# Kernel tuning notes

Hardware: AMD Instinct MI355X
Metric: run time of the kernel (lower is better)

Reference implementation:

```python
import jax, jax.numpy as jnp
import numpy as np

D = 256      # feature_dim (d_model)
H = 4        # num_heads
N = 4096     # query nodes
M = 4096     # source nodes


def _conv1x1(W, b, x):
    # Conv1d(kernel_size=1): per-position linear over channels. x: [1, Cin, N]
    return jnp.einsum('oi,bin->bon', W, x) + b[None, :, None]


def setup_inputs() -> dict:
    key = jax.random.key(0)
    ks = jax.random.split(key, 16)
    s = 0.02
    inp = {
        'x':      jax.random.normal(ks[0], (1, D, N), jnp.float32),
        'source': jax.random.normal(ks[1], (1, D, M), jnp.float32),
        'dist':   jax.random.uniform(ks[2], (1, N, M), jnp.float32),
        'mask':   jax.random.bernoulli(ks[3], 0.5, (N, M)),
        'Wq': s * jax.random.normal(ks[4], (D, D), jnp.float32),  'bq': jnp.zeros((D,), jnp.float32),
        'Wk': s * jax.random.normal(ks[5], (D, D), jnp.float32),  'bk': jnp.zeros((D,), jnp.float32),
        'Wv': s * jax.random.normal(ks[6], (D, D), jnp.float32),  'bv': jnp.zeros((D,), jnp.float32),
        'Wm': s * jax.random.normal(ks[7], (D, D), jnp.float32),  'bm': jnp.zeros((D,), jnp.float32),
        'W1': s * jax.random.normal(ks[8], (2 * D, 2 * D), jnp.float32), 'b1': jnp.zeros((2 * D,), jnp.float32),
        'W2': s * jax.random.normal(ks[9], (D, 2 * D), jnp.float32),     'b2': jnp.zeros((D,), jnp.float32),
    }
    return inp


def reference(x, source, dist, mask, Wq, bq, Wk, bk, Wv, bv, Wm, bm, W1, b1, W2, b2):
    dim = D // H  # per-head dim; torch view(1, dim, H, -1) splits channels as (dim, H)
    q = _conv1x1(Wq, bq, x).reshape(1, dim, H, N)
    k = _conv1x1(Wk, bk, source).reshape(1, dim, H, M)
    v = _conv1x1(Wv, bv, source).reshape(1, dim, H, M)

    scores = jnp.einsum('bdhn,bdhm->bhnm', q, k) / jnp.sqrt(jnp.asarray(dim, q.dtype))
    # non-standard additive mask: global detached min scales the masked-out entries
    smin = jax.lax.stop_gradient(scores.min())
    scores = scores + smin * (~mask).astype(scores.dtype)[None, None, :, :]

    prob = jax.nn.softmax(scores, axis=-1)                       # [1,H,N,M]
    attn = jnp.einsum('bhnm,bdhm->bdhn', prob, v)                # [1,dim,H,N]
    message = _conv1x1(Wm, bm, attn.reshape(1, D, N))            # merge heads

    h = jnp.concatenate([x, message], axis=1)                    # [1,2D,N]
    h = jax.nn.relu(_conv1x1(W1, b1, h))
    y = _conv1x1(W2, b2, h)                                      # [1,D,N]
    weights = scores.mean(axis=1)                                # [1,N,M]
    return y, weights
```

## Files before the change

kernel.cpp:

```cpp
#include <hip/hip_runtime.h>
#include <hip/hip_bf16.h>
#include <math.h>

#define Dm 256
#define Hh 4
#define Nn 4096
#define Mq 4096

typedef __attribute__((ext_vector_type(8))) short bf16x8;
typedef __attribute__((ext_vector_type(4))) float f32x4;
typedef _Float16 __attribute__((ext_vector_type(4))) f16x4;

#define MFMA_BF16(a,b,c) __builtin_amdgcn_mfma_f32_16x16x32_bf16(a,b,c,0,0,0)
#define MFMA_F16x16(a,b,c) __builtin_amdgcn_mfma_f32_16x16x16f16(a,b,c,0,0,0)

#define MB (1u<<20)
#define OFF_FLAG  0
#define OFF_SMIN  64
#define OFF_PART  128
#define OFF_MT    4096
#define OFF_DENP  (128u<<10)
#define OFF_STATS (512u<<10)
#define OFF_WB    (3u*MB/2)
#define OFF_BITS  (3u*MB)
#define OFF_QB    (5u*MB)
#define OFF_KB    (7u*MB)
#define OFF_VB    (9u*MB)
#define OFF_HCAT  (11u*MB)
#define OFF_ATTNT (15u*MB)
#define OFF_XT    (17u*MB)
#define OFF_ST    (19u*MB)
#define OFF_OPART (17u*MB)
#define OFF_H1T   (17u*MB)

#define WOFF_Q  0
#define WOFF_K  65536
#define WOFF_V  131072
#define WOFF_M  196608
#define WOFF_1  262144
#define WOFF_2  524288

__device__ __forceinline__ unsigned short f2bf(float x) {
    unsigned u = __float_as_uint(x);
    u += 0x7FFF + ((u >> 16) & 1);
    return (unsigned short)(u >> 16);
}
__device__ __forceinline__ float bf2f(unsigned short b) {
    return __uint_as_float(((unsigned)b) << 16);
}

__global__ void k_detect(const unsigned char* __restrict__ mb, int* __restrict__ flag) {
    __shared__ int c[5];
    if (threadIdx.x < 5) c[threadIdx.x] = 0;
    __syncthreads();
    for (int i = threadIdx.x; i < 16384; i += blockDim.x) {
        unsigned char b = mb[i];
        if (b) {
            atomicAdd(&c[i & 3], 1);
            if ((i & 7) == 4) atomicAdd(&c[4], 1);
        }
    }
    __syncthreads();
    if (threadIdx.x == 0) {
        int f;
        if (c[3] > 0 && c[0] == 0)          f = 3;
        else if (c[1] | c[2] | c[3])        f = 1;
        else if (c[4] > 0)                  f = 0;
        else                                f = 2;
        *flag = f;
    }
}

__global__ void k_maskbits(const void* __restrict__ mp, const int* __restrict__ flagp,
                           unsigned char* __restrict__ bits) {
    size_t i = (size_t)blockIdx.x * 256 + threadIdx.x;
    const int flag = *flagp;
    size_t base = i * 8;
    unsigned b = 0;
    if (flag == 1) {
        unsigned long long u = *(const unsigned long long*)((const unsigned char*)mp + base);
        #pragma unroll
        for (int j = 0; j < 8; j++) b |= (unsigned)(((u >> (8*j)) & 0xFFull) != 0ull) << j;
    } else if (flag == 0) {
        const int* p = (const int*)mp;
        #pragma unroll
        for (int j = 0; j < 8; j++) b |= (unsigned)(p[base + j] != 0) << j;
    } else if (flag == 3) {
        const float* p = (const float*)mp;
        #pragma unroll
        for (int j = 0; j < 8; j++) b |= (unsigned)(p[base + j] != 0.0f) << j;
    } else {
        const unsigned long long* p = (const unsigned long long*)mp;
        #pragma unroll
        for (int j = 0; j < 8; j++) b |= (unsigned)(p[base + j] != 0ull) << j;
    }
    bits[i] = (unsigned char)b;
}

__global__ __launch_bounds__(256) void k_prep(const float* __restrict__ src,
                                              unsigned short* __restrict__ dst,
                                              unsigned short* __restrict__ dst2) {
    const int l = threadIdx.x & 63, g = threadIdx.x >> 6;
    const int c = blockIdx.y * 64 + l;
    const int n0 = blockIdx.x * 32 + g * 8;
    float4 v0 = *(const float4*)(src + (size_t)c * Nn + n0);
    float4 v1 = *(const float4*)(src + (size_t)c * Nn + n0 + 4);
    float vv[8] = {v0.x, v0.y, v0.z, v0.w, v1.x, v1.y, v1.z, v1.w};
    #pragma unroll
    for (int j = 0; j < 8; j++) {
        unsigned short b = f2bf(vv[j]);
        dst[(size_t)(n0 + j) * 256 + c] = b;
        if (dst2) dst2[(size_t)(n0 + j) * 512 + c] = b;
    }
}

__global__ void k_wcast(const float* __restrict__ Wq, const float* __restrict__ Wk,
                        const float* __restrict__ Wv, const float* __restrict__ Wm,
                        const float* __restrict__ W1, const float* __restrict__ W2,
                        unsigned short* __restrict__ wb) {
    size_t i = (size_t)blockIdx.x * 256 + threadIdx.x;
    const float* s; size_t off;
    if      (i < 65536)               { s = Wq; off = i; }
    else if (i < 131072)              { s = Wk; off = i - 65536; }
    else if (i < 196608)              { s = Wv; off = i - 131072; }
    else if (i < 262144)              { s = Wm; off = i - 196608; }
    else if (i < 524288)              { s = W1; off = i - 262144; }
    else                              { s = W2; off = i - 524288; }
    wb[i] = f2bf(s[off]);
}

template<int KK>
__device__ __forceinline__ void gemm_body(const unsigned short* __restrict__ wb,
                                          const float* __restrict__ bias,
                                          const unsigned short* __restrict__ xt,
                                          void* __restrict__ out, int mode,
                                          int bx, int by) {
    const int tid = threadIdx.x, w = tid >> 6, lane = tid & 63;
    const int lg = lane >> 4, lr = lane & 15;
    const int o_base = by * 64 + w * 16;
    const int n_base = bx * 64;
    f32x4 acc[4];
    #pragma unroll
    for (int j = 0; j < 4; j++) acc[j] = (f32x4){0.f, 0.f, 0.f, 0.f};
    const unsigned short* wrow = wb + (size_t)(o_base + lr) * KK + lg * 8;
    const unsigned short* xrow = xt + (size_t)(n_base + lr) * KK + lg * 8;
    #pragma unroll
    for (int k0 = 0; k0 < KK; k0 += 32) {
        bf16x8 af = *(const bf16x8*)(wrow + k0);
        #pragma unroll
        for (int j = 0; j < 4; j++) {
            bf16x8 bfr = *(const bf16x8*)(xrow + (size_t)j * 16 * KK + k0);
            acc[j] = MFMA_BF16(af, bfr, acc[j]);
        }
    }
    float bv[4];
    #pragma unroll
    for (int r = 0; r < 4; r++) bv[r] = bias[o_base + lg * 4 + r];
    #pragma unroll
    for (int j = 0; j < 4; j++) {
        #pragma unroll
        for (int r = 0; r < 4; r++) {
            int o = o_base + lg * 4 + r;
            int n = n_base + j * 16 + lr;
            float v = acc[j][r] + bv[r];
            if (mode == 0) {
                ((float*)out)[(size_t)o * Nn + n] = v;
            } else if (mode == 1) {
                ((unsigned short*)out)[(((size_t)(o & 3)) * Nn + n) * 64 + (o >> 2)] = f2bf(v);
            } else if (mode == 2) {
                union { _Float16 h; unsigned short u; } cv; cv.h = (_Float16)v;
                ((unsigned short*)out)[(((size_t)(o & 3)) * 64 + (o >> 2)) * Mq + n] = cv.u;
            } else if (mode == 3) {
                ((unsigned short*)out)[(size_t)n * 512 + 256 + o] = f2bf(v);
            } else if (mode == 4) {
                ((unsigned short*)out)[(size_t)n * 512 + o] = f2bf(fmaxf(v, 0.f));
            } else {
                int dd = o >> 2, hh = o & 3, g = dd >> 3, pos = dd & 7;
                int slot = g ^ (n & 7);
                ((unsigned short*)out)[(((size_t)hh * Mq + n)) * 64 + slot * 8 + pos] = f2bf(v);
            }
        }
    }
}

template<int KK>
__global__ __launch_bounds__(256) void k_mgemm(const unsigned short* __restrict__ wb,
                                               const float* __restrict__ bias,
                                               const unsigned short* __restrict__ xt,
                                               void* __restrict__ out, int mode) {
    gemm_body<KK>(wb, bias, xt, out, mode, blockIdx.x, blockIdx.y);
}

__global__ __launch_bounds__(256) void k_qkv(const unsigned short* __restrict__ wb,
                                             const float* __restrict__ bq,
                                             const float* __restrict__ bk,
                                             const float* __restrict__ bv,
                                             const unsigned short* __restrict__ xt,
                                             const unsigned short* __restrict__ st,
                                             void* __restrict__ qb, void* __restrict__ kb,
                                             void* __restrict__ vb) {
    const int z = blockIdx.z;
    const float* bias = (z == 0) ? bq : ((z == 1) ? bk : bv);
    const unsigned short* X = (z == 0) ? xt : st;
    void* out = (z == 0) ? qb : ((z == 1) ? kb : vb);
    int mode = (z == 0) ? 1 : ((z == 1) ? 5 : 2);
    gemm_body<256>(wb + z * 65536, bias, X, out, mode, blockIdx.x, blockIdx.y);
}

template<int PHASE>
__global__ __launch_bounds__(512) void k_score(
    const unsigned short* __restrict__ qb, const unsigned short* __restrict__ kb,
    const unsigned long long* __restrict__ bits,
    const float* __restrict__ sminp,
    float* __restrict__ stats, float* __restrict__ partial,
    float* __restrict__ wout) {
    __shared__ unsigned short kbuf[2][8192];
    const int tid = threadIdx.x;
    const int w = tid >> 6, lane = tid & 63;
    const int lg = lane >> 4, lr = lane & 15;
    const int n0 = blockIdx.x * 128 + w * 16;
    const int mb = blockIdx.y;
    const int m0 = mb * 512;

    bf16x8 qf[4][2];
    #pragma unroll
    for (int h = 0; h < 4; h++)
        #pragma unroll
        for (int kh = 0; kh < 2; kh++)
            qf[h][kh] = *(const bf16x8*)(qb + (((size_t)h * Nn + n0 + lr) << 6) + kh*32 + lg*8);

    float smin = 0.f;
    if (PHASE) smin = *sminp;

    const int h0 = tid >> 8, q0 = tid & 255;
    const unsigned short* src0 = kb + (((size_t)h0 * Mq + m0) << 6) + q0 * 8;
    const unsigned short* src1 = kb + (((size_t)(h0 + 2) * Mq + m0) << 6) + q0 * 8;
    unsigned short* dst0 = &kbuf[0][h0 * 2048 + q0 * 8];
    unsigned short* dst1 = &kbuf[0][(h0 + 2) * 2048 + q0 * 8];

    float mn = INFINITY;
    float mx1[4], mx0[4];
    #pragma unroll
    for (int h = 0; h < 4; h++) { mx1[h] = -INFINITY; mx0[h] = -INFINITY; }

    const unsigned long long* brow = bits + (((size_t)(n0 + lr)) << 6) + (m0 >> 6);
    unsigned long long bw = 0ull;

    bf16x8 r0 = *(const bf16x8*)(src0);
    bf16x8 r1 = *(const bf16x8*)(src1);
    *(bf16x8*)dst0 = r0;
    *(bf16x8*)dst1 = r1;
    __syncthreads();
    r0 = *(const bf16x8*)(src0 + 2048);
    r1 = *(const bf16x8*)(src1 + 2048);

    for (int t = 0; t < 16; t++) {
        const unsigned short* kB = &kbuf[t & 1][0];
        const int mch = m0 + t * 32;
        if ((t & 1) == 0) bw = brow[t >> 1];
        #pragma unroll
        for (int mi = 0; mi < 2; mi++) {
            const int rowoff = (mi * 16 + lr) * 64;
            const int shb = (t & 1) * 32 + mi * 16 + lg * 4;
            f32x4 ssum = (f32x4){0.f, 0.f, 0.f, 0.f};
            #pragma unroll
            for (int h = 0; h < 4; h++) {
                bf16x8 a0 = *(const bf16x8*)(kB + h*2048 + rowoff + ((lg ^ (lr & 7)) << 3));
                bf16x8 a1 = *(const bf16x8*)(kB + h*2048 + rowoff + (((lg + 4) ^ (lr & 7)) << 3));
                f32x4 acc = (f32x4){0.f, 0.f, 0.f, 0.f};
                acc = MFMA_BF16(a0, qf[h][0], acc);
                acc = MFMA_BF16(a1, qf[h][1], acc);
                if (PHASE == 0) {
                    #pragma unroll
                    for (int r = 0; r < 4; r++) {
                        float v = acc[r] * 0.125f;
                        mn = fminf(mn, v);
                        bool b = (bw >> (shb + r)) & 1ull;
                        mx1[h] = fmaxf(mx1[h], b ? v : -INFINITY);
                        mx0[h] = fmaxf(mx0[h], b ? -INFINITY : v);
                    }
                } else {
                    ssum += acc;
                }
            }
            if (PHASE == 1) {
                f32x4 wv;
                #pragma unroll
                for (int r = 0; r < 4; r++) {
                    bool b = (bw >> (shb + r)) & 1ull;
                    wv[r] = ssum[r] * 0.03125f + (b ? 0.f : smin);
                }
                *(f32x4*)(wout + (size_t)(n0 + lr) * Mq + mch + mi * 16 + lg * 4) = wv;
            }
        }
        if (t < 15) {
            *(bf16x8*)(dst0 + (((t + 1) & 1) ? 8192 : 0)) = r0;
            *(bf16x8*)(dst1 + (((t + 1) & 1) ? 8192 : 0)) = r1;
        }
        __syncthreads();
        if (t < 14) {
            r0 = *(const bf16x8*)(src0 + (size_t)(t + 2) * 2048);
            r1 = *(const bf16x8*)(src1 + (size_t)(t + 2) * 2048);
        }
    }

    if (PHASE == 0) {
        #pragma unroll
        for (int h = 0; h < 4; h++) {
            mx1[h] = fmaxf(mx1[h], __shfl_xor(mx1[h], 16));
            mx1[h] = fmaxf(mx1[h], __shfl_xor(mx1[h], 32));
            mx0[h] = fmaxf(mx0[h], __shfl_xor(mx0[h], 16));
            mx0[h] = fmaxf(mx0[h], __shfl_xor(mx0[h], 32));
        }
        if (lane < 16) {
            #pragma unroll
            for (int h = 0; h < 4; h++) {
                size_t row = (size_t)h * Nn + n0 + lane;
                stats[row * 16 + mb * 2 + 0] = mx1[h];
                stats[row * 16 + mb * 2 + 1] = mx0[h];
            }
        }
        for (int off = 1; off < 64; off <<= 1) mn = fminf(mn, __shfl_xor(mn, off));
        __shared__ float wmin[8];
        if (lane == 0) wmin[w] = mn;
        __syncthreads();
        if (tid == 0) {
            float m2 = wmin[0];
            #pragma unroll
            for (int i = 1; i < 8; i++) m2 = fminf(m2, wmin[i]);
            partial[blockIdx.x * 8 + mb] = m2;
        }
    }
}

__global__ void k_minreduce(const float* __restrict__ partial, float* __restrict__ smin) {
    const int tid = threadIdx.x;
    float mn = partial[tid];
    __shared__ float red[256];
    red[tid] = mn;
    __syncthreads();
    for (int st = 128; st > 0; st >>= 1) {
        if (tid < st) red[tid] = fminf(red[tid], red[tid + st]);
        __syncthreads();
    }
    if (tid == 0) *smin = red[0];
}

__global__ void k_rowfix(const float* __restrict__ stats, const float* __restrict__ sminp,
                         float* __restrict__ mtarr) {
    int row = blockIdx.x * 256 + threadIdx.x;
    float smin = *sminp;
    float mt = -INFINITY;
    #pragma unroll
    for (int mb = 0; mb < 8; mb++) {
        float a = stats[(size_t)row * 16 + mb * 2];
        float b = stats[(size_t)row * 16 + mb * 2 + 1];
        mt = fmaxf(mt, fmaxf(a, b + smin));
    }
    mtarr[row] = mt;
}

__global__ __launch_bounds__(512) void k_pv(
    const unsigned short* __restrict__ qb, const unsigned short* __restrict__ kb,
    const unsigned short* __restrict__ vbh,
    const unsigned long long* __restrict__ bits,
    const float* __restrict__ sminp, const float* __restrict__ mtarr,
    float* __restrict__ denp, unsigned short* __restrict__ opart) {
    __shared__ unsigned short kbuf[2][4096];
    const int tid = threadIdx.x;
    const int w = tid >> 6, lane = tid & 63;
    const int lg = lane >> 4, lr = lane & 15;
    const int h = blockIdx.y & 3, mb = (blockIdx.y >> 2) & 3, dh = blockIdx.y >> 4;
    const int n0 = blockIdx.x * 512 + w * 64;
    const int m0 = mb * 1024;
    const float smin = *sminp;

    bf16x8 qf[4][2];
    float mt[4];
    #pragma unroll
    for (int ns = 0; ns < 4; ns++) {
        #pragma unroll
        for (int kh = 0; kh < 2; kh++)
            qf[ns][kh] = *(const bf16x8*)(qb + (((size_t)h * Nn + n0 + ns*16 + lr) << 6) + kh*32 + lg*8);
        mt[ns] = mtarr[(size_t)h * Nn + n0 + ns*16 + lr];
    }

    f32x4 oacc[4][2];
    float dsum[4];
    #pragma unroll
    for (int ns = 0; ns < 4; ns++) {
        oacc[ns][0] = (f32x4){0.f,0.f,0.f,0.f};
        oacc[ns][1] = (f32x4){0.f,0.f,0.f,0.f};
        dsum[ns] = 0.f;
    }

    const unsigned short* ksrc = kb + (((size_t)h * Mq + m0) << 6) + tid * 8;
    bf16x8 r0 = *(const bf16x8*)(ksrc);
    *(bf16x8*)&kbuf[0][tid * 8] = r0;
    __syncthreads();
    r0 = *(const bf16x8*)(ksrc + 4096);

    const unsigned short* vrow0 = vbh + ((size_t)(h * 64 + dh * 32 + lr)) * Mq;
    const unsigned short* vrow1 = vbh + ((size_t)(h * 64 + dh * 32 + 16 + lr)) * Mq;

    for (int t = 0; t < 16; t++) {
        const unsigned short* kB = &kbuf[t & 1][0];
        const int mch = m0 + t * 64;
        unsigned long long bw[4];
        #pragma unroll
        for (int ns = 0; ns < 4; ns++)
            bw[ns] = bits[(((size_t)(n0 + ns*16 + lr)) << 6) + (mch >> 6)];
        #pragma unroll
        for (int mi = 0; mi < 4; mi++) {
            const int rowoff = (mi * 16 + lr) * 64;
            bf16x8 a0 = *(const bf16x8*)(kB + rowoff + ((lg ^ (lr & 7)) << 3));
            bf16x8 a1 = *(const bf16x8*)(kB + rowoff + (((lg + 4) ^ (lr & 7)) << 3));
            f16x4 vf0 = *(const f16x4*)(vrow0 + mch + mi * 16 + lg * 4);
            f16x4 vf1 = *(const f16x4*)(vrow1 + mch + mi * 16 + lg * 4);
            const int shb = mi * 16 + lg * 4;
            #pragma unroll
            for (int ns = 0; ns < 4; ns++) {
                f32x4 acc = (f32x4){0.f,0.f,0.f,0.f};
                acc = MFMA_BF16(a0, qf[ns][0], acc);
                acc = MFMA_BF16(a1, qf[ns][1], acc);
                f16x4 pf;
                float dloc = 0.f;
                #pragma unroll
                for (int r = 0; r < 4; r++) {
                    bool b = (bw[ns] >> (shb + r)) & 1ull;
                    float v = acc[r] * 0.125f + (b ? 0.f : smin);
                    float p = __expf(v - mt[ns]);
                    dloc += p;
                    pf[r] = (_Float16)p;
                }
                dsum[ns] += dloc;
                oacc[ns][0] = MFMA_F16x16(pf, vf0, oacc[ns][0]);
                oacc[ns][1] = MFMA_F16x16(pf, vf1, oacc[ns][1]);
            }
        }
        if (t < 15) *(bf16x8*)&kbuf[(t + 1) & 1][tid * 8] = r0;
        __syncthreads();
        if (t < 14) r0 = *(const bf16x8*)(ksrc + (size_t)(t + 2) * 4096);
    }

    #pragma unroll
    for (int ns = 0; ns < 4; ns++) {
        dsum[ns] += __shfl_xor(dsum[ns], 16);
        dsum[ns] += __shfl_xor(dsum[ns], 32);
    }
    if (dh == 0 && lane < 16) {
        #pragma unroll
        for (int ns = 0; ns < 4; ns++)
            denp[((size_t)h * Nn + n0 + ns*16 + lane) * 4 + mb] = dsum[ns];
    }
    unsigned short* op = opart + (size_t)mb * (Dm * Nn);
    #pragma unroll
    for (int ns = 0; ns < 4; ns++)
        #pragma unroll
        for (int ds = 0; ds < 2; ds++) {
            int c = (dh * 32 + ds * 16 + lr) * 4 + h;
            int n = n0 + ns * 16 + lg * 4;
            unsigned long long pk =
                (unsigned long long)f2bf(oacc[ns][ds][0]) |
                ((unsigned long long)f2bf(oacc[ns][ds][1]) << 16) |
                ((unsigned long long)f2bf(oacc[ns][ds][2]) << 32) |
                ((unsigned long long)f2bf(oacc[ns][ds][3]) << 48);
            *(unsigned long long*)&op[(size_t)c * Nn + n] = pk;
        }
}

__global__ __launch_bounds__(256) void k_finish(const unsigned short* __restrict__ opart,
                                                const float* __restrict__ denp,
                                                unsigned short* __restrict__ attnT) {
    __shared__ float t[64][65];
    const int cb = blockIdx.y * 64, nb = blockIdx.x * 64;
    const int tid = threadIdx.x;
    #pragma unroll
    for (int e = 0; e < 16; e++) {
        int idx = e * 256 + tid;
        int c_l = idx >> 6, n_l = idx & 63;
        int c = cb + c_l, n = nb + n_l;
        float s = 0.f;
        #pragma unroll
        for (int y = 0; y < 4; y++)
            s += bf2f(opart[(size_t)y * (Dm*Nn) + (size_t)c * Nn + n]);
        size_t row = (size_t)(c & 3) * Nn + n;
        float d = denp[row*4] + denp[row*4+1] + denp[row*4+2] + denp[row*4+3];
        t[c_l][n_l] = s / d;
    }
    __syncthreads();
    #pragma unroll
    for (int e = 0; e < 16; e++) {
        int idx = e * 256 + tid;
        int n_l = idx >> 6, c_l = idx & 63;
        attnT[(size_t)(nb + n_l) * 256 + cb + c_l] = f2bf(t[c_l][n_l]);
    }
}

extern "C" void kernel_launch(void* const* d_in, const int* in_sizes, int n_in,
                              void* d_out, int out_size, void* d_ws, size_t ws_size,
                              hipStream_t stream) {
    const float* x      = (const float*)d_in[0];
    const float* source = (const float*)d_in[1];
    const void*  mask   = d_in[3];
    const float* Wq = (const float*)d_in[4];  const float* bq = (const float*)d_in[5];
    const float* Wk = (const float*)d_in[6];  const float* bk = (const float*)d_in[7];
    const float* Wv = (const float*)d_in[8];  const float* bv = (const float*)d_in[9];
    const float* Wm = (const float*)d_in[10]; const float* bm = (const float*)d_in[11];
    const float* W1 = (const float*)d_in[12]; const float* b1 = (const float*)d_in[13];
    const float* W2 = (const float*)d_in[14]; const float* b2 = (const float*)d_in[15];

    float* y    = (float*)d_out;
    float* wout = y + (size_t)Dm * Nn;

    char* ws = (char*)d_ws;
    int*   flag  = (int*)(ws + OFF_FLAG);
    float* sminp = (float*)(ws + OFF_SMIN);
    float* part  = (float*)(ws + OFF_PART);
    float* mtarr = (float*)(ws + OFF_MT);
    float* denp  = (float*)(ws + OFF_DENP);
    float* stats = (float*)(ws + OFF_STATS);
    unsigned short* wb    = (unsigned short*)(ws + OFF_WB);
    unsigned char*  bits  = (unsigned char*)(ws + OFF_BITS);
    unsigned short* qb    = (unsigned short*)(ws + OFF_QB);
    unsigned short* kb    = (unsigned short*)(ws + OFF_KB);
    unsigned short* vb    = (unsigned short*)(ws + OFF_VB);
    unsigned short* hcat  = (unsigned short*)(ws + OFF_HCAT);
    unsigned short* attnT = (unsigned short*)(ws + OFF_ATTNT);
    unsigned short* xt    = (unsigned short*)(ws + OFF_XT);
    unsigned short* st    = (unsigned short*)(ws + OFF_ST);
    unsigned short* opart = (unsigned short*)(ws + OFF_OPART);
    unsigned short* h1t   = (unsigned short*)(ws + OFF_H1T);

    k_detect<<<1, 256, 0, stream>>>((const unsigned char*)mask, flag);
    k_maskbits<<<8192, 256, 0, stream>>>(mask, flag, bits);

    k_prep<<<dim3(128, 4), 256, 0, stream>>>(x, xt, hcat);
    k_prep<<<dim3(128, 4), 256, 0, stream>>>(source, st, nullptr);
    k_wcast<<<2560, 256, 0, stream>>>(Wq, Wk, Wv, Wm, W1, W2, wb);

    k_qkv<<<dim3(64, 4, 3), 256, 0, stream>>>(wb, bq, bk, bv, xt, st, qb, kb, vb);

    k_score<0><<<dim3(32, 8), 512, 0, stream>>>(qb, kb, (const unsigned long long*)bits,
                                                nullptr, stats, part, nullptr);
    k_minreduce<<<1, 256, 0, stream>>>(part, sminp);
    k_rowfix<<<64, 256, 0, stream>>>(stats, sminp, mtarr);

    k_score<1><<<dim3(32, 8), 512, 0, stream>>>(qb, kb, (const unsigned long long*)bits,
                                                sminp, nullptr, nullptr, wout);

    k_pv<<<dim3(8, 32), 512, 0, stream>>>(qb, kb, vb, (const unsigned long long*)bits,
                                          sminp, mtarr, denp, opart);
    k_finish<<<dim3(64, 4), 256, 0, stream>>>(opart, denp, attnT);

    k_mgemm<256><<<dim3(64, 4), 256, 0, stream>>>(wb + WOFF_M, bm, attnT, hcat, 3);
    k_mgemm<512><<<dim3(64, 8), 256, 0, stream>>>(wb + WOFF_1, b1, hcat, h1t, 4);
    k_mgemm<512><<<dim3(64, 4), 256, 0, stream>>>(wb + WOFF_2, b2, h1t, y, 0);
}
```

Measured before the change: 235.3 us.

## Replace exact row max with Cauchy-Schwarz bound and stage V in LDS

The exact per-row softmax max is no longer computed from masked score statistics. It is replaced by a Cauchy-Schwarz upper bound, |q|·max|k|/8 plus a clamped smin, computed by small norm kernels. This removes the stats output and the row-fix kernel and makes the min pass lighter. The PV kernel is restructured to stage V tiles through double-buffered LDS, cover all 64 head dims per block, and fold scale and offset into an exp2 FMA. The bound may underflow exponents when it is loose, which trades accuracy risk for fewer passes over the score matrix.

```diff
diff --git a/kernel.cpp b/kernel.cpp
--- a/kernel.cpp
+++ b/kernel.cpp
@@ -18,9 +18,9 @@
 #define OFF_FLAG  0
 #define OFF_SMIN  64
 #define OFF_PART  128
+#define OFF_KMAX  2048
 #define OFF_MT    4096
 #define OFF_DENP  (128u<<10)
-#define OFF_STATS (512u<<10)
 #define OFF_WB    (3u*MB/2)
 #define OFF_BITS  (3u*MB)
 #define OFF_QB    (5u*MB)
@@ -207,20 +207,49 @@
     gemm_body<256>(wb + z * 65536, bias, X, out, mode, blockIdx.x, blockIdx.y);
 }
 
-template<int PHASE>
-__global__ __launch_bounds__(512) void k_score(
+__global__ void k_init(unsigned* __restrict__ kmax) {
+    if (threadIdx.x < 4) kmax[threadIdx.x] = 0u;
+}
+
+__global__ __launch_bounds__(256) void k_knorm(const unsigned short* __restrict__ kb,
+                                               unsigned* __restrict__ kmax) {
+    const int h = blockIdx.y;
+    const int m = blockIdx.x * 256 + threadIdx.x;
+    const unsigned short* row = kb + ((size_t)(h * Mq + m) << 6);
+    float s = 0.f;
+    #pragma unroll
+    for (int i = 0; i < 64; i++) { float v = bf2f(row[i]); s = fmaf(v, v, s); }
+    __shared__ float red[256];
+    red[threadIdx.x] = s;
+    __syncthreads();
+    for (int st = 128; st > 0; st >>= 1) {
+        if (threadIdx.x < st) red[threadIdx.x] = fmaxf(red[threadIdx.x], red[threadIdx.x + st]);
+        __syncthreads();
+    }
+    if (threadIdx.x == 0) atomicMax(kmax + h, __float_as_uint(red[0]));
+}
+
+__global__ __launch_bounds__(256) void k_qnorm(const unsigned short* __restrict__ qb,
+                                               const unsigned* __restrict__ kmax,
+                                               float* __restrict__ mtarr) {
+    const int row = blockIdx.x * 256 + threadIdx.x;
+    const unsigned short* qr = qb + ((size_t)row << 6);
+    float s = 0.f;
+    #pragma unroll
+    for (int i = 0; i < 64; i++) { float v = bf2f(qr[i]); s = fmaf(v, v, s); }
+    float k2 = __uint_as_float(kmax[row >> 12]);
+    mtarr[row] = sqrtf(s * k2) * 0.125f;
+}
+
+__global__ __launch_bounds__(512) void k_min(
     const unsigned short* __restrict__ qb, const unsigned short* __restrict__ kb,
-    const unsigned long long* __restrict__ bits,
-    const float* __restrict__ sminp,
-    float* __restrict__ stats, float* __restrict__ partial,
-    float* __restrict__ wout) {
+    float* __restrict__ partial) {
     __shared__ unsigned short kbuf[2][8192];
     const int tid = threadIdx.x;
     const int w = tid >> 6, lane = tid & 63;
     const int lg = lane >> 4, lr = lane & 15;
     const int n0 = blockIdx.x * 128 + w * 16;
-    const int mb = blockIdx.y;
-    const int m0 = mb * 512;
+    const int m0 = blockIdx.y * 512;
 
     bf16x8 qf[4][2];
     #pragma unroll
@@ -228,9 +257,6 @@
         #pragma unroll
         for (int kh = 0; kh < 2; kh++)
             qf[h][kh] = *(const bf16x8*)(qb + (((size_t)h * Nn + n0 + lr) << 6) + kh*32 + lg*8);
-
-    float smin = 0.f;
-    if (PHASE) smin = *sminp;
 
     const int h0 = tid >> 8, q0 = tid & 255;
     const unsigned short* src0 = kb + (((size_t)h0 * Mq + m0) << 6) + q0 * 8;
@@ -239,12 +265,6 @@
     unsigned short* dst1 = &kbuf[0][(h0 + 2) * 2048 + q0 * 8];
 
     float mn = INFINITY;
-    float mx1[4], mx0[4];
-    #pragma unroll
-    for (int h = 0; h < 4; h++) { mx1[h] = -INFINITY; mx0[h] = -INFINITY; }
-
-    const unsigned long long* brow = bits + (((size_t)(n0 + lr)) << 6) + (m0 >> 6);
-    unsigned long long bw = 0ull;
 
     bf16x8 r0 = *(const bf16x8*)(src0);
     bf16x8 r1 = *(const bf16x8*)(src1);
@@ -256,13 +276,9 @@
 
     for (int t = 0; t < 16; t++) {
         const unsigned short* kB = &kbuf[t & 1][0];
-        const int mch = m0 + t * 32;
-        if ((t & 1) == 0) bw = brow[t >> 1];
         #pragma unroll
         for (int mi = 0; mi < 2; mi++) {
             const int rowoff = (mi * 16 + lr) * 64;
-            const int shb = (t & 1) * 32 + mi * 16 + lg * 4;
-            f32x4 ssum = (f32x4){0.f, 0.f, 0.f, 0.f};
             #pragma unroll
             for (int h = 0; h < 4; h++) {
                 bf16x8 a0 = *(const bf16x8*)(kB + h*2048 + rowoff + ((lg ^ (lr & 7)) << 3));
@@ -270,27 +286,7 @@
                 f32x4 acc = (f32x4){0.f, 0.f, 0.f, 0.f};
                 acc = MFMA_BF16(a0, qf[h][0], acc);
                 acc = MFMA_BF16(a1, qf[h][1], acc);
-                if (PHASE == 0) {
-                    #pragma unroll
-                    for (int r = 0; r < 4; r++) {
-                        float v = acc[r] * 0.125f;
-                        mn = fminf(mn, v);
-                        bool b = (bw >> (shb + r)) & 1ull;
-                        mx1[h] = fmaxf(mx1[h], b ? v : -INFINITY);
-                        mx0[h] = fmaxf(mx0[h], b ? -INFINITY : v);
-                    }
-                } else {
-                    ssum += acc;
-                }
-            }
-            if (PHASE == 1) {
-                f32x4 wv;
-                #pragma unroll
-                for (int r = 0; r < 4; r++) {
-                    bool b = (bw >> (shb + r)) & 1ull;
-                    wv[r] = ssum[r] * 0.03125f + (b ? 0.f : smin);
-                }
-                *(f32x4*)(wout + (size_t)(n0 + lr) * Mq + mch + mi * 16 + lg * 4) = wv;
+                mn = fminf(mn, fminf(fminf(acc[0], acc[1]), fminf(acc[2], acc[3])));
             }
         }
         if (t < 15) {
@@ -304,32 +300,15 @@
         }
     }
 
-    if (PHASE == 0) {
-        #pragma unroll
-        for (int h = 0; h < 4; h++) {
-            mx1[h] = fmaxf(mx1[h], __shfl_xor(mx1[h], 16));
-            mx1[h] = fmaxf(mx1[h], __shfl_xor(mx1[h], 32));
-            mx0[h] = fmaxf(mx0[h], __shfl_xor(mx0[h], 16));
-            mx0[h] = fmaxf(mx0[h], __shfl_xor(mx0[h], 32));
-        }
-        if (lane < 16) {
-            #pragma unroll
-            for (int h = 0; h < 4; h++) {
-                size_t row = (size_t)h * Nn + n0 + lane;
-                stats[row * 16 + mb * 2 + 0] = mx1[h];
-                stats[row * 16 + mb * 2 + 1] = mx0[h];
-            }
-        }
-        for (int off = 1; off < 64; off <<= 1) mn = fminf(mn, __shfl_xor(mn, off));
-        __shared__ float wmin[8];
-        if (lane == 0) wmin[w] = mn;
-        __syncthreads();
-        if (tid == 0) {
-            float m2 = wmin[0];
-            #pragma unroll
-            for (int i = 1; i < 8; i++) m2 = fminf(m2, wmin[i]);
-            partial[blockIdx.x * 8 + mb] = m2;
-        }
+    for (int off = 1; off < 64; off <<= 1) mn = fminf(mn, __shfl_xor(mn, off));
+    __shared__ float wmin[8];
+    if (lane == 0) wmin[w] = mn;
+    __syncthreads();
+    if (tid == 0) {
+        float m2 = wmin[0];
+        #pragma unroll
+        for (int i = 1; i < 8; i++) m2 = fminf(m2, wmin[i]);
+        partial[blockIdx.x * 8 + blockIdx.y] = m2 * 0.125f;
     }
 }
 
@@ -346,18 +325,84 @@
     if (tid == 0) *smin = red[0];
 }
 
-__global__ void k_rowfix(const float* __restrict__ stats, const float* __restrict__ sminp,
-                         float* __restrict__ mtarr) {
-    int row = blockIdx.x * 256 + threadIdx.x;
-    float smin = *sminp;
-    float mt = -INFINITY;
-    #pragma unroll
-    for (int mb = 0; mb < 8; mb++) {
-        float a = stats[(size_t)row * 16 + mb * 2];
-        float b = stats[(size_t)row * 16 + mb * 2 + 1];
-        mt = fmaxf(mt, fmaxf(a, b + smin));
-    }
-    mtarr[row] = mt;
+__global__ __launch_bounds__(512) void k_wout(
+    const unsigned short* __restrict__ qb, const unsigned short* __restrict__ kb,
+    const unsigned long long* __restrict__ bits,
+    const float* __restrict__ sminp, float* __restrict__ wout) {
+    __shared__ unsigned short kbuf[2][8192];
+    const int tid = threadIdx.x;
+    const int w = tid >> 6, lane = tid & 63;
+    const int lg = lane >> 4, lr = lane & 15;
+    const int n0 = blockIdx.x * 128 + w * 16;
+    const int m0 = blockIdx.y * 512;
+    const float smin = *sminp;
+
+    bf16x8 qf[4][2];
+    #pragma unroll
+    for (int h = 0; h < 4; h++)
+        #pragma unroll
+        for (int kh = 0; kh < 2; kh++)
+            qf[h][kh] = *(const bf16x8*)(qb + (((size_t)h * Nn + n0 + lr) << 6) + kh*32 + lg*8);
+
+    const int h0 = tid >> 8, q0 = tid & 255;
+    const unsigned short* src0 = kb + (((size_t)h0 * Mq + m0) << 6) + q0 * 8;
+    const unsigned short* src1 = kb + (((size_t)(h0 + 2) * Mq + m0) << 6) + q0 * 8;
+    unsigned short* dst0 = &kbuf[0][h0 * 2048 + q0 * 8];
+    unsigned short* dst1 = &kbuf[0][(h0 + 2) * 2048 + q0 * 8];
+
+    const unsigned long long* brow = bits + (((size_t)(n0 + lr)) << 6) + (m0 >> 6);
+    unsigned long long bw = 0ull;
+
+    bf16x8 r0 = *(const bf16x8*)(src0);
+    bf16x8 r1 = *(const bf16x8*)(src1);
+    *(bf16x8*)dst0 = r0;
+    *(bf16x8*)dst1 = r1;
+    __syncthreads();
+    r0 = *(const bf16x8*)(src0 + 2048);
+    r1 = *(const bf16x8*)(src1 + 2048);
+
+    for (int t = 0; t < 16; t++) {
+        const unsigned short* kB = &kbuf[t & 1][0];
+        const int mch = m0 + t * 32;
+        if ((t & 1) == 0) bw = brow[t >> 1];
+        #pragma unroll
+        for (int mi = 0; mi < 2; mi++) {
+            const int rowoff = (mi * 16 + lr) * 64;
+            f32x4 accA = (f32x4){0.f, 0.f, 0.f, 0.f};
+            f32x4 accB = (f32x4){0.f, 0.f, 0.f, 0.f};
+            #pragma unroll
+            for (int h = 0; h < 2; h++) {
+                bf16x8 a0 = *(const bf16x8*)(kB + h*2048 + rowoff + ((lg ^ (lr & 7)) << 3));
+                bf16x8 a1 = *(const bf16x8*)(kB + h*2048 + rowoff + (((lg + 4) ^ (lr & 7)) << 3));
+                accA = MFMA_BF16(a0, qf[h][0], accA);
+                accA = MFMA_BF16(a1, qf[h][1], accA);
+            }
+            #pragma unroll
+            for (int h = 2; h < 4; h++) {
+                bf16x8 a0 = *(const bf16x8*)(kB + h*2048 + rowoff + ((lg ^ (lr & 7)) << 3));
+                bf16x8 a1 = *(const bf16x8*)(kB + h*2048 + rowoff + (((lg + 4) ^ (lr & 7)) << 3));
+                accB = MFMA_BF16(a0, qf[h][0], accB);
+                accB = MFMA_BF16(a1, qf[h][1], accB);
+            }
+            const int shb = (t & 1) * 32 + mi * 16 + lg * 4;
+            f32x4 wv;
+            #pragma unroll
+            for (int r = 0; r < 4; r++) {
+                bool b = (bw >> (shb + r)) & 1ull;
+                wv[r] = fmaf(accA[r] + accB[r], 0.03125f, b ? 0.f : smin);
+            }
+            *(f32x4*)(wout + (size_t)(n0 + lr) * Mq + mch + mi * 16 + lg * 4) = wv;
+        }
+        if (t < 15) {
+            *(bf16x8*)(dst0 + (((t + 1) & 1) ? 8192 : 0)) = r0;
+            *(bf16x8*)(dst1 + (((t + 1) & 1) ? 8192 : 0)) = r1;
+        }
+        __syncthreads();
+        if (t < 14) {
+            r0 = *(const bf16x8*)(src0 + (size_t)(t + 2) * 2048);
+            r1 = *(const bf16x8*)(src1 + (size_t)(t + 2) * 2048);
+        }
+    }
 }
 
 __global__ __launch_bounds__(512) void k_pv(
@@ -367,60 +412,70 @@
     const float* __restrict__ sminp, const float* __restrict__ mtarr,
     float* __restrict__ denp, unsigned short* __restrict__ opart) {
     __shared__ unsigned short kbuf[2][4096];
+    __shared__ unsigned short vbuf[2][4096];
     const int tid = threadIdx.x;
     const int w = tid >> 6, lane = tid & 63;
     const int lg = lane >> 4, lr = lane & 15;
-    const int h = blockIdx.y & 3, mb = (blockIdx.y >> 2) & 3, dh = blockIdx.y >> 4;
-    const int n0 = blockIdx.x * 512 + w * 64;
+    const int h = blockIdx.y & 3, mb = blockIdx.y >> 2;
+    const int n0 = blockIdx.x * 256 + w * 32;
     const int m0 = mb * 1024;
     const float smin = *sminp;
-
-    bf16x8 qf[4][2];
-    float mt[4];
-    #pragma unroll
-    for (int ns = 0; ns < 4; ns++) {
+    const float sminc = fmaxf(smin, 0.f);
+
+    bf16x8 qf[2][2];
+    float cT[2], cF[2];
+    #pragma unroll
+    for (int ns = 0; ns < 2; ns++) {
         #pragma unroll
         for (int kh = 0; kh < 2; kh++)
             qf[ns][kh] = *(const bf16x8*)(qb + (((size_t)h * Nn + n0 + ns*16 + lr) << 6) + kh*32 + lg*8);
-        mt[ns] = mtarr[(size_t)h * Nn + n0 + ns*16 + lr];
-    }
-
-    f32x4 oacc[4][2];
-    float dsum[4];
-    #pragma unroll
-    for (int ns = 0; ns < 4; ns++) {
-        oacc[ns][0] = (f32x4){0.f,0.f,0.f,0.f};
-        oacc[ns][1] = (f32x4){0.f,0.f,0.f,0.f};
-        dsum[ns] = 0.f;
-    }
+        float mtE = mtarr[(size_t)h * Nn + n0 + ns*16 + lr] + sminc;
+        cT[ns] = -mtE * 1.44269504f;
+        cF[ns] = cT[ns] + smin * 1.44269504f;
+    }
+
+    f32x4 oacc[2][4];
+    #pragma unroll
+    for (int ns = 0; ns < 2; ns++)
+        #pragma unroll
+        for (int ds = 0; ds < 4; ds++)
+            oacc[ns][ds] = (f32x4){0.f, 0.f, 0.f, 0.f};
+    float dsum[2] = {0.f, 0.f};
 
     const unsigned short* ksrc = kb + (((size_t)h * Mq + m0) << 6) + tid * 8;
-    bf16x8 r0 = *(const bf16x8*)(ksrc);
-    *(bf16x8*)&kbuf[0][tid * 8] = r0;
-    __syncthreads();
-    r0 = *(const bf16x8*)(ksrc + 4096);
-
-    const unsigned short* vrow0 = vbh + ((size_t)(h * 64 + dh * 32 + lr)) * Mq;
-    const unsigned short* vrow1 = vbh + ((size_t)(h * 64 + dh * 32 + 16 + lr)) * Mq;
+    const int vj = tid & 7, vdd = tid >> 3;
+    const unsigned short* vsrc = vbh + (size_t)(h * 64 + vdd) * Mq + m0 + vj * 8;
+    const int vdst = ((vj >> 1) * 64 + vdd) * 16 + (vj & 1) * 8;
+
+    bf16x8 rk = *(const bf16x8*)(ksrc);
+    bf16x8 rv = *(const bf16x8*)(vsrc);
+    *(bf16x8*)&kbuf[0][tid * 8] = rk;
+    *(bf16x8*)&vbuf[0][vdst] = rv;
+    __syncthreads();
+    rk = *(const bf16x8*)(ksrc + 4096);
+    rv = *(const bf16x8*)(vsrc + 64);
 
     for (int t = 0; t < 16; t++) {
         const unsigned short* kB = &kbuf[t & 1][0];
+        const unsigned short* vB = &vbuf[t & 1][0];
         const int mch = m0 + t * 64;
-        unsigned long long bw[4];
-        #pragma unroll
-        for (int ns = 0; ns < 4; ns++)
+        unsigned long long bw[2];
+        #pragma unroll
+        for (int ns = 0; ns < 2; ns++)
             bw[ns] = bits[(((size_t)(n0 + ns*16 + lr)) << 6) + (mch >> 6)];
         #pragma unroll
         for (int mi = 0; mi < 4; mi++) {
             const int rowoff = (mi * 16 + lr) * 64;
             bf16x8 a0 = *(const bf16x8*)(kB + rowoff + ((lg ^ (lr & 7)) << 3));
             bf16x8 a1 = *(const bf16x8*)(kB + rowoff + (((lg + 4) ^ (lr & 7)) << 3));
-            f16x4 vf0 = *(const f16x4*)(vrow0 + mch + mi * 16 + lg * 4);
-            f16x4 vf1 = *(const f16x4*)(vrow1 + mch + mi * 16 + lg * 4);
+            f16x4 vf[4];
+            #pragma unroll
+            for (int ds = 0; ds < 4; ds++)
+                vf[ds] = *(const f16x4*)&vB[(mi * 64 + ds * 16 + lr) * 16 + lg * 4];
             const int shb = mi * 16 + lg * 4;
             #pragma unroll
-            for (int ns = 0; ns < 4; ns++) {
-                f32x4 acc = (f32x4){0.f,0.f,0.f,0.f};
+            for (int ns = 0; ns < 2; ns++) {
+                f32x4 acc = (f32x4){0.f, 0.f, 0.f, 0.f};
                 acc = MFMA_BF16(a0, qf[ns][0], acc);
                 acc = MFMA_BF16(a1, qf[ns][1], acc);
                 f16x4 pf;
@@ -428,37 +483,43 @@
                 #pragma unroll
                 for (int r = 0; r < 4; r++) {
                     bool b = (bw[ns] >> (shb + r)) & 1ull;
-                    float v = acc[r] * 0.125f + (b ? 0.f : smin);
-                    float p = __expf(v - mt[ns]);
+                    float p = exp2f(fmaf(acc[r], 0.18033688f, b ? cT[ns] : cF[ns]));
                     dloc += p;
                     pf[r] = (_Float16)p;
                 }
                 dsum[ns] += dloc;
-                oacc[ns][0] = MFMA_F16x16(pf, vf0, oacc[ns][0]);
-                oacc[ns][1] = MFMA_F16x16(pf, vf1, oacc[ns][1]);
+                #pragma unroll
+                for (int ds = 0; ds < 4; ds++)
+                    oacc[ns][ds] = MFMA_F16x16(pf, vf[ds], oacc[ns][ds]);
             }
         }
-        if (t < 15) *(bf16x8*)&kbuf[(t + 1) & 1][tid * 8] = r0;
+        if (t < 15) {
+            *(bf16x8*)&kbuf[(t + 1) & 1][tid * 8] = rk;
+            *(bf16x8*)&vbuf[(t + 1) & 1][vdst] = rv;
+        }
         __syncthreads();
-        if (t < 14) r0 = *(const bf16x8*)(ksrc + (size_t)(t + 2) * 4096);
-    }
-
-    #pragma unroll
-    for (int ns = 0; ns < 4; ns++) {
+        if (t < 14) {
+            rk = *(const bf16x8*)(ksrc + (size_t)(t + 2) * 4096);
+            rv = *(const bf16x8*)(vsrc + (size_t)(t + 2) * 64);
+        }
+    }
+
+    #pragma unroll
+    for (int ns = 0; ns < 2; ns++) {
         dsum[ns] += __shfl_xor(dsum[ns], 16);
         dsum[ns] += __shfl_xor(dsum[ns], 32);
     }
-    if (dh == 0 && lane < 16) {
-        #pragma unroll
-        for (int ns = 0; ns < 4; ns++)
+    if (lane < 16) {
+        #pragma unroll
+        for (int ns = 0; ns < 2; ns++)
             denp[((size_t)h * Nn + n0 + ns*16 + lane) * 4 + mb] = dsum[ns];
     }
     unsigned short* op = opart + (size_t)mb * (Dm * Nn);
     #pragma unroll
-    for (int ns = 0; ns < 4; ns++)
-        #pragma unroll
-        for (int ds = 0; ds < 2; ds++) {
-            int c = (dh * 32 + ds * 16 + lr) * 4 + h;
+    for (int ns = 0; ns < 2; ns++)
+        #pragma unroll
+        for (int ds = 0; ds < 4; ds++) {
+            int c = (ds * 16 + lr) * 4 + h;
             int n = n0 + ns * 16 + lg * 4;
             unsigned long long pk =
                 (unsigned long long)f2bf(oacc[ns][ds][0]) |
@@ -514,12 +575,12 @@
     float* wout = y + (size_t)Dm * Nn;
 
     char* ws = (char*)d_ws;
-    int*   flag  = (int*)(ws + OFF_FLAG);
-    float* sminp = (float*)(ws + OFF_SMIN);
-    float* part  = (float*)(ws + OFF_PART);
-    float* mtarr = (float*)(ws + OFF_MT);
-    float* denp  = (float*)(ws + OFF_DENP);
-    float* stats = (float*)(ws + OFF_STATS);
+    int*      flag  = (int*)(ws + OFF_FLAG);
+    float*    sminp = (float*)(ws + OFF_SMIN);
+    float*    part  = (float*)(ws + OFF_PART);
+    unsigned* kmax  = (unsigned*)(ws + OFF_KMAX);
+    float*    mtarr = (float*)(ws + OFF_MT);
+    float*    denp  = (float*)(ws + OFF_DENP);
     unsigned short* wb    = (unsigned short*)(ws + OFF_WB);
     unsigned char*  bits  = (unsigned char*)(ws + OFF_BITS);
     unsigned short* qb    = (unsigned short*)(ws + OFF_QB);
@@ -541,16 +602,17 @@
 
     k_qkv<<<dim3(64, 4, 3), 256, 0, stream>>>(wb, bq, bk, bv, xt, st, qb, kb, vb);
 
-    k_score<0><<<dim3(32, 8), 512, 0, stream>>>(qb, kb, (const unsigned long long*)bits,
-                                                nullptr, stats, part, nullptr);
+    k_init<<<1, 64, 0, stream>>>(kmax);
+    k_knorm<<<dim3(16, 4), 256, 0, stream>>>(kb, kmax);
+    k_qnorm<<<64, 256, 0, stream>>>(qb, kmax, mtarr);
+
+    k_min<<<dim3(32, 8), 512, 0, stream>>>(qb, kb, part);
     k_minreduce<<<1, 256, 0, stream>>>(part, sminp);
-    k_rowfix<<<64, 256, 0, stream>>>(stats, sminp, mtarr);
-
-    k_score<1><<<dim3(32, 8), 512, 0, stream>>>(qb, kb, (const unsigned long long*)bits,
-                                                sminp, nullptr, nullptr, wout);
-
-    k_pv<<<dim3(8, 32), 512, 0, stream>>>(qb, kb, vb, (const unsigned long long*)bits,
-                                          sminp, mtarr, denp, opart);
+
+    k_wout<<<dim3(32, 8), 512, 0, stream>>>(qb, kb, (const unsigned long long*)bits, sminp, wout);
+
+    k_pv<<<dim3(16, 16), 512, 0, stream>>>(qb, kb, vb, (const unsigned long long*)bits,
+                                           sminp, mtarr, denp, opart);
     k_finish<<<dim3(64, 4), 256, 0, stream>>>(opart, denp, attnT);
 
     k_mgemm<256><<<dim3(64, 4), 256, 0, stream>>>(wb + WOFF_M, bm, attnT, hcat, 3);
```

Measured after the change: 208.1 us. -11.5%, faster.
